# Performance work log

Measured on AMD Instinct MI355X. Metric: run time of the kernel, lower is better.

Reference implementation:

```python
import jax, jax.numpy as jnp
import numpy as np
from jax import lax


def _conv(x, w, b):
    # NCHW x OIHW, stride 1, VALID padding (matches nn.Conv2d padding=0)
    y = lax.conv_general_dilated(x, w, (1, 1), 'VALID',
                                 dimension_numbers=('NCHW', 'OIHW', 'NCHW'))
    return y + b[None, :, None, None]


def _maxpool2(x):
    return lax.reduce_window(x, -jnp.inf, lax.max, (1, 1, 2, 2), (1, 1, 2, 2), 'VALID')


def setup_inputs() -> dict:
    key = jax.random.key(0)
    ks = jax.random.split(key, 8)
    B, C, H, W = 4096, 3, 32, 32
    E, NC = 8, 1000  # out_dim (=n learners), num_classes
    inp = {
        'x': jax.random.normal(ks[0], (B, C, H, W), jnp.float32),
        'conv1_w': jax.random.normal(ks[1], (1, 3, 5, 5), jnp.float32) * 0.1,
        'conv1_b': jnp.zeros((1,), jnp.float32),
        'conv2_w': jax.random.normal(ks[2], (2, 1, 5, 5), jnp.float32) * 0.1,
        'conv2_b': jnp.zeros((2,), jnp.float32),
        'conv3_w': jax.random.normal(ks[3], (4, 2, 5, 5), jnp.float32) * 0.1,
        'conv3_b': jnp.zeros((4,), jnp.float32),
        'fc_w': jax.random.normal(ks[4], (E, 4), jnp.float32) * 0.5,
        'fc_b': jnp.zeros((E,), jnp.float32),
        'ens_w': jax.random.normal(ks[5], (E, C * H * W, NC), jnp.float32) * 0.02,
        'ens_b': jnp.zeros((E, NC), jnp.float32),
        'k': 2,
    }
    return inp


def reference(x, conv1_w, conv1_b, conv2_w, conv2_b, conv3_w, conv3_b,
              fc_w, fc_b, ens_w, ens_b, k):
    B = x.shape[0]
    # --- selector CNN stem ---
    h = jax.nn.relu(_conv(x, conv1_w, conv1_b))   # [B,1,28,28]
    h = _maxpool2(h)                              # [B,1,14,14]
    h = jax.nn.relu(_conv(h, conv2_w, conv2_b))   # [B,2,10,10]
    h = _maxpool2(h)                              # [B,2,5,5]
    h = jax.nn.relu(_conv(h, conv3_w, conv3_b))   # [B,4,1,1]
    h = h.reshape(B, -1)                          # [B,4]
    z = h @ fc_w.T + fc_b                         # [B,E]
    # L2NormalizationLayer with clamp(min=1e-9)
    z = z / jnp.clip(jnp.linalg.norm(z, axis=-1, keepdims=True), 1e-9, None)
    # TopK -> one-hot routing mask (straight-through style forward)
    _, idx = lax.top_k(z, k)                      # [B,k]
    mask = jax.nn.one_hot(idx, z.shape[-1], dtype=z.dtype).sum(-2)  # [B,E] in {0,1}
    # --- frozen ensemble: linear weak learners, combined via mask ---
    xf = x.reshape(B, -1)                          # [B,F]
    outs = jnp.einsum('bf,efc->bec', xf, ens_w) + ens_b[None]  # [B,E,NC]
    return (outs * mask[:, :, None]).sum(axis=1)   # [B,NC]
```

## Files before the change

kernel.cpp:

```cpp
#include <hip/hip_runtime.h>
#include <hip/hip_bf16.h>
#include <stdint.h>

#define B_SZ 4096
#define F_SZ 3072
#define NCLS 1000
#define NE 8
#define NPAD 1024
#define CAP 4096

#define OFF_CNT   0
#define OFF_LIST  1024
#define OFF_PAIR  132096
#define OFF_XB    262144
#define OFF_WT    25427968

typedef unsigned short u16;
typedef __attribute__((ext_vector_type(8))) short short8v;
typedef __attribute__((ext_vector_type(4))) float f32x4;

__device__ __forceinline__ u16 f2bf(float f) {
  unsigned int u = __float_as_uint(f);
  u = (u + 0x7FFFu + ((u >> 16) & 1u)) >> 16;
  return (u16)u;
}

__device__ __forceinline__ void gll16(const void* g, void* l) {
  __builtin_amdgcn_global_load_lds(
      (const __attribute__((address_space(1))) void*)g,
      (__attribute__((address_space(3))) void*)l, 16, 0, 0);
}

__global__ __launch_bounds__(256) void transpose_w(const float* __restrict__ ensw,
                                                   u16* __restrict__ wt) {
  __shared__ u16 tile[64 * 68];
  int t = threadIdx.x;
  int n0 = blockIdx.x * 64, k0 = blockIdx.y * 64, e = blockIdx.z;
  const float* src = ensw + (size_t)e * (F_SZ * NCLS);
  int kr = t >> 4, nq = (t & 15) * 4;
  for (int it = 0; it < 4; ++it) {
    int kk = kr + it * 16;
    const float* sp = src + (size_t)(k0 + kk) * NCLS + n0 + nq;
    float4 v;
    if (n0 + nq + 3 < NCLS) v = *(const float4*)sp;
    else {
      v.x = (n0 + nq     < NCLS) ? sp[0] : 0.f;
      v.y = (n0 + nq + 1 < NCLS) ? sp[1] : 0.f;
      v.z = (n0 + nq + 2 < NCLS) ? sp[2] : 0.f;
      v.w = (n0 + nq + 3 < NCLS) ? sp[3] : 0.f;
    }
    u16* d = tile + kk * 68 + nq;
    d[0] = f2bf(v.x); d[1] = f2bf(v.y); d[2] = f2bf(v.z); d[3] = f2bf(v.w);
  }
  __syncthreads();
  int rn = t >> 3, c8 = t & 7;
  for (int it = 0; it < 2; ++it) {
    int n = rn + it * 32;
    u16 o[8];
#pragma unroll
    for (int jj = 0; jj < 8; ++jj) o[jj] = tile[(c8 * 8 + jj) * 68 + n];
    uint4 pk;
    pk.x = (unsigned)o[0] | ((unsigned)o[1] << 16);
    pk.y = (unsigned)o[2] | ((unsigned)o[3] << 16);
    pk.z = (unsigned)o[4] | ((unsigned)o[5] << 16);
    pk.w = (unsigned)o[6] | ((unsigned)o[7] << 16);
    *(uint4*)(wt + ((size_t)(e * NPAD + n0 + n)) * F_SZ + k0 + c8 * 8) = pk;
  }
}

__global__ __launch_bounds__(128) void selector(
    const float* __restrict__ x,
    const float* __restrict__ w1, const float* __restrict__ b1,
    const float* __restrict__ w2, const float* __restrict__ b2,
    const float* __restrict__ w3, const float* __restrict__ b3,
    const float* __restrict__ fw, const float* __restrict__ fb,
    u16* __restrict__ xb16, int* __restrict__ cnt, int* __restrict__ list,
    int* __restrict__ expair) {
  __shared__ float wgt[384];
  __shared__ float S[2][4352];
  int t = threadIdx.x;
  for (int i = t; i < 372; i += 128) {
    float v;
    if      (i <  75) v = w1[i];
    else if (i <  76) v = b1[i - 75];
    else if (i < 126) v = w2[i - 76];
    else if (i < 128) v = b2[i - 126];
    else if (i < 328) v = w3[i - 128];
    else if (i < 332) v = b3[i - 328];
    else if (i < 364) v = fw[i - 332];
    else              v = fb[i - 364];
    wgt[i] = v;
  }
  int w = t >> 6, l = t & 63;
  int b = blockIdx.x * 2 + w;
  float* xs   = S[w];
  float* buf1 = xs + 3072;
  float* p1   = xs + 3856;
  float* buf2 = xs + 4052;
  float* p2   = xs + 4252;
  float* hb   = xs + 4302;
  float* zb   = xs + 4306;

  const float4* gx = (const float4*)(x + (size_t)b * F_SZ);
  float4* xs4 = (float4*)xs;
  ushort4* gxb = (ushort4*)(xb16 + (size_t)b * F_SZ);
  for (int it = 0; it < 12; ++it) {
    int idx = it * 64 + l;
    float4 v = gx[idx];
    xs4[idx] = v;
    ushort4 h4;
    h4.x = f2bf(v.x); h4.y = f2bf(v.y); h4.z = f2bf(v.z); h4.w = f2bf(v.w);
    gxb[idx] = h4;
  }
  __syncthreads();

  if (l < 56) {
    int y = l >> 1, xh = l & 1;
    float acc[14];
#pragma unroll
    for (int xc = 0; xc < 14; ++xc) acc[xc] = wgt[75];
    for (int c = 0; c < 3; ++c)
      for (int i = 0; i < 5; ++i) {
        const float4* rb = (const float4*)(xs + c * 1024 + (y + i) * 32) + xh * 3;
        float a[20];
#pragma unroll
        for (int q = 0; q < 5; ++q) {
          float4 v = rb[q];
          a[q * 4] = v.x; a[q * 4 + 1] = v.y; a[q * 4 + 2] = v.z; a[q * 4 + 3] = v.w;
        }
        if (xh) {
#pragma unroll
          for (int q = 0; q < 18; ++q) a[q] = a[q + 2];
        }
        const float* wp = wgt + c * 25 + i * 5;
        float W0 = wp[0], W1 = wp[1], W2 = wp[2], W3 = wp[3], W4 = wp[4];
#pragma unroll
        for (int xc = 0; xc < 14; ++xc)
          acc[xc] += a[xc] * W0 + a[xc + 1] * W1 + a[xc + 2] * W2 + a[xc + 3] * W3 + a[xc + 4] * W4;
      }
#pragma unroll
    for (int xc = 0; xc < 14; ++xc) buf1[y * 28 + xh * 14 + xc] = fmaxf(acc[xc], 0.f);
  }
  __syncthreads();

  for (int it = 0; it < 4; ++it) {
    int p = it * 64 + l;
    if (p < 196) {
      int py = p / 14, px = p % 14;
      const float* r0 = buf1 + (2 * py) * 28 + 2 * px;
      p1[p] = fmaxf(fmaxf(r0[0], r0[1]), fmaxf(r0[28], r0[29]));
    }
  }
  __syncthreads();

  for (int it = 0; it < 4; ++it) {
    int p = it * 64 + l;
    if (p < 200) {
      int o = p / 100, rem = p % 100, yy = rem / 10, xx = rem % 10;
      float acc = wgt[126 + o];
      const float* wp = wgt + 76 + o * 25;
      for (int i = 0; i < 5; ++i)
#pragma unroll
        for (int j = 0; j < 5; ++j) acc += p1[(yy + i) * 14 + xx + j] * wp[i * 5 + j];
      buf2[p] = fmaxf(acc, 0.f);
    }
  }
  __syncthreads();

  if (l < 50) {
    int o = l / 25, rem = l % 25, yy = rem / 5, xx = rem % 5;
    const float* r0 = buf2 + o * 100 + (2 * yy) * 10 + 2 * xx;
    p2[l] = fmaxf(fmaxf(r0[0], r0[1]), fmaxf(r0[10], r0[11]));
  }
  __syncthreads();

  if (l < 4) {
    float acc = wgt[328 + l];
    const float* wp = wgt + 128 + l * 50;
    for (int cc = 0; cc < 50; ++cc) acc += p2[cc] * wp[cc];
    hb[l] = fmaxf(acc, 0.f);
  }
  __syncthreads();

  if (l < 8) {
    float acc = wgt[364 + l];
    const float* wp = wgt + 332 + l * 4;
#pragma unroll
    for (int j = 0; j < 4; ++j) acc += hb[j] * wp[j];
    zb[l] = acc;
  }
  __syncthreads();

  if (l == 0) {
    float zz[8];
#pragma unroll
    for (int e = 0; e < 8; ++e) zz[e] = zb[e];
    int e1 = 0; float v1 = zz[0];
    for (int e = 1; e < 8; ++e) if (zz[e] > v1) { v1 = zz[e]; e1 = e; }
    int e2 = -1; float v2 = 0.f;
    for (int e = 0; e < 8; ++e) {
      if (e == e1) continue;
      if (e2 < 0 || zz[e] > v2) { v2 = zz[e]; e2 = e; }
    }
    int p1i = atomicAdd(&cnt[e1], 1); list[e1 * CAP + p1i] = b;
    int p2i = atomicAdd(&cnt[e2], 1); list[e2 * CAP + p2i] = b;
    expair[b] = e1 | (e2 << 8);
  }
}

__global__ __launch_bounds__(256) void bias_init(const int* __restrict__ expair,
                                                 const float* __restrict__ ensb,
                                                 float* __restrict__ out) {
  int b = blockIdx.x;
  int pr = expair[b];
  const float* p1 = ensb + (size_t)(pr & 255) * NCLS;
  const float* p2 = ensb + (size_t)((pr >> 8) & 255) * NCLS;
  float* op = out + (size_t)b * NCLS;
  for (int c = threadIdx.x; c < NCLS; c += 256) op[c] = p1[c] + p2[c];
}

__global__ __launch_bounds__(256) void moe_gemm(const u16* __restrict__ xb,
                                                const u16* __restrict__ wt,
                                                const int* __restrict__ cnt,
                                                const int* __restrict__ list,
                                                float* __restrict__ out) {
  __shared__ u16 As[128 * 32];
  __shared__ u16 Bs[128 * 32];
  __shared__ int idx_s[128];
  int e = blockIdx.z;
  int cnt_e = cnt[e];
  int m0 = blockIdx.y * 128;
  if (m0 >= cnt_e) return;
  int n0 = blockIdx.x * 128;
  int t = threadIdx.x;
  const int* lst = list + e * CAP;
  if (t < 128) {
    int m = m0 + t;
    idx_s[t] = lst[min(m, cnt_e - 1)];
  }
  __syncthreads();

  int rA1 = t >> 2,        sA1 = (t & 3) ^ ((rA1 >> 1) & 3);
  int rA2 = 64 + (t >> 2), sA2 = (t & 3) ^ ((rA2 >> 1) & 3);
  size_t ia1 = (size_t)idx_s[rA1], ia2 = (size_t)idx_s[rA2];
  const u16* pA1 = xb + ia1 * F_SZ + sA1 * 8;
  const u16* pA2 = xb + ia2 * F_SZ + sA2 * 8;
  const u16* pB1 = wt + ((size_t)(e * NPAD) + n0 + rA1) * F_SZ + sA1 * 8;
  const u16* pB2 = wt + ((size_t)(e * NPAD) + n0 + rA2) * F_SZ + sA2 * 8;
  u16* dA1 = As + t * 8;
  u16* dA2 = As + (t + 256) * 8;
  u16* dB1 = Bs + t * 8;
  u16* dB2 = Bs + (t + 256) * 8;

  int w = t >> 6, l = t & 63;
  int lr = l & 15, hk = l >> 4;
  int wrow = (w >> 1) * 64, wcol = (w & 1) * 64;
  const short8v* fA[4];
  const short8v* fB[4];
#pragma unroll
  for (int i = 0; i < 4; ++i) {
    int ra = wrow + i * 16 + lr;
    fA[i] = (const short8v*)(As + ra * 32 + (hk ^ ((ra >> 1) & 3)) * 8);
    int rb = wcol + i * 16 + lr;
    fB[i] = (const short8v*)(Bs + rb * 32 + (hk ^ ((rb >> 1) & 3)) * 8);
  }

  f32x4 acc[4][4] = {};
  for (int k0 = 0; k0 < F_SZ; k0 += 32) {
    __syncthreads();
    gll16(pA1, dA1); gll16(pA2, dA2);
    gll16(pB1, dB1); gll16(pB2, dB2);
    pA1 += 32; pA2 += 32; pB1 += 32; pB2 += 32;
    __syncthreads();
    short8v av[4], bv[4];
#pragma unroll
    for (int i = 0; i < 4; ++i) av[i] = *fA[i];
#pragma unroll
    for (int j = 0; j < 4; ++j) bv[j] = *fB[j];
#pragma unroll
    for (int i = 0; i < 4; ++i)
#pragma unroll
      for (int j = 0; j < 4; ++j)
        acc[i][j] = __builtin_amdgcn_mfma_f32_16x16x32_bf16(av[i], bv[j], acc[i][j], 0, 0, 0);
  }

#pragma unroll
  for (int i = 0; i < 4; ++i) {
#pragma unroll
    for (int r = 0; r < 4; ++r) {
      int mt = wrow + i * 16 + hk * 4 + r;
      if (m0 + mt < cnt_e) {
        float* orow = out + (size_t)idx_s[mt] * NCLS;
#pragma unroll
        for (int j = 0; j < 4; ++j) {
          int col = n0 + wcol + j * 16 + lr;
          if (col < NCLS) unsafeAtomicAdd(orow + col, acc[i][j][r]);
        }
      }
    }
  }
}

extern "C" void kernel_launch(void* const* d_in, const int* in_sizes, int n_in,
                              void* d_out, int out_size, void* d_ws, size_t ws_size,
                              hipStream_t stream) {
  const float* x   = (const float*)d_in[0];
  const float* w1  = (const float*)d_in[1];
  const float* b1  = (const float*)d_in[2];
  const float* w2  = (const float*)d_in[3];
  const float* b2  = (const float*)d_in[4];
  const float* w3  = (const float*)d_in[5];
  const float* b3  = (const float*)d_in[6];
  const float* fw  = (const float*)d_in[7];
  const float* fb  = (const float*)d_in[8];
  const float* ensw = (const float*)d_in[9];
  const float* ensb = (const float*)d_in[10];
  float* out = (float*)d_out;

  uint8_t* ws = (uint8_t*)d_ws;
  int* cnt    = (int*)(ws + OFF_CNT);
  int* list   = (int*)(ws + OFF_LIST);
  int* expair = (int*)(ws + OFF_PAIR);
  u16* xb16   = (u16*)(ws + OFF_XB);
  u16* wt     = (u16*)(ws + OFF_WT);

  hipMemsetAsync(cnt, 0, 64, stream);
  transpose_w<<<dim3(16, 48, 8), 256, 0, stream>>>(ensw, wt);
  selector<<<2048, 128, 0, stream>>>(x, w1, b1, w2, b2, w3, b3, fw, fb,
                                     xb16, cnt, list, expair);
  bias_init<<<4096, 256, 0, stream>>>(expair, ensb, out);
  moe_gemm<<<dim3(8, 32, 8), 256, 0, stream>>>(xb16, wt, cnt, list, out);
}
```

Baseline: 470.9 us.

## Double-buffer MoE GEMM with BK=64, pad selector smem rows, vectorize bias init

The MoE GEMM now keeps two LDS buffers with a K-tile of 64 and an XOR swizzle over 8 chunks. Global-to-LDS loads for the next stage are issued before the MFMAs on the current stage, and there is one barrier per iteration instead of two. The selector pads each image row to 36 floats in shared memory to reduce bank conflicts in the conv1 reads. Bias init switches to float4 loads and stores. The larger LDS footprint (64KB per GEMM block) may reduce occupancy.

```diff
diff --git a/kernel.cpp b/kernel.cpp
--- a/kernel.cpp
+++ b/kernel.cpp
@@ -68,6 +68,8 @@
   }
 }
 
+#define XST 36
+#define XCH 1152
 __global__ __launch_bounds__(128) void selector(
     const float* __restrict__ x,
     const float* __restrict__ w1, const float* __restrict__ b1,
@@ -77,7 +79,7 @@
     u16* __restrict__ xb16, int* __restrict__ cnt, int* __restrict__ list,
     int* __restrict__ expair) {
   __shared__ float wgt[384];
-  __shared__ float S[2][4352];
+  __shared__ float S[2][4704];
   int t = threadIdx.x;
   for (int i = t; i < 372; i += 128) {
     float v;
@@ -94,20 +96,21 @@
   int w = t >> 6, l = t & 63;
   int b = blockIdx.x * 2 + w;
   float* xs   = S[w];
-  float* buf1 = xs + 3072;
-  float* p1   = xs + 3856;
-  float* buf2 = xs + 4052;
-  float* p2   = xs + 4252;
-  float* hb   = xs + 4302;
-  float* zb   = xs + 4306;
+  float* buf1 = xs + 3456;
+  float* p1   = xs + 4240;
+  float* buf2 = xs + 4436;
+  float* p2   = xs + 4636;
+  float* hb   = xs + 4686;
+  float* zb   = xs + 4690;
 
   const float4* gx = (const float4*)(x + (size_t)b * F_SZ);
-  float4* xs4 = (float4*)xs;
   ushort4* gxb = (ushort4*)(xb16 + (size_t)b * F_SZ);
   for (int it = 0; it < 12; ++it) {
     int idx = it * 64 + l;
     float4 v = gx[idx];
-    xs4[idx] = v;
+    int f = idx * 4;
+    int c = f >> 10, rem = f & 1023, y = rem >> 5, xc = rem & 31;
+    *(float4*)(xs + c * XCH + y * XST + xc) = v;
     ushort4 h4;
     h4.x = f2bf(v.x); h4.y = f2bf(v.y); h4.z = f2bf(v.z); h4.w = f2bf(v.w);
     gxb[idx] = h4;
@@ -121,7 +124,7 @@
     for (int xc = 0; xc < 14; ++xc) acc[xc] = wgt[75];
     for (int c = 0; c < 3; ++c)
       for (int i = 0; i < 5; ++i) {
-        const float4* rb = (const float4*)(xs + c * 1024 + (y + i) * 32) + xh * 3;
+        const float4* rb = (const float4*)(xs + c * XCH + (y + i) * XST) + xh * 3;
         float a[20];
 #pragma unroll
         for (int q = 0; q < 5; ++q) {
@@ -212,11 +215,15 @@
                                                  const float* __restrict__ ensb,
                                                  float* __restrict__ out) {
   int b = blockIdx.x;
+  int t = threadIdx.x;
+  if (t >= 250) return;
   int pr = expair[b];
-  const float* p1 = ensb + (size_t)(pr & 255) * NCLS;
-  const float* p2 = ensb + (size_t)((pr >> 8) & 255) * NCLS;
-  float* op = out + (size_t)b * NCLS;
-  for (int c = threadIdx.x; c < NCLS; c += 256) op[c] = p1[c] + p2[c];
+  const float4* p1 = (const float4*)(ensb + (size_t)(pr & 255) * NCLS);
+  const float4* p2 = (const float4*)(ensb + (size_t)((pr >> 8) & 255) * NCLS);
+  float4* op = (float4*)(out + (size_t)b * NCLS);
+  float4 a = p1[t], c = p2[t];
+  float4 r; r.x = a.x + c.x; r.y = a.y + c.y; r.z = a.z + c.z; r.w = a.w + c.w;
+  op[t] = r;
 }
 
 __global__ __launch_bounds__(256) void moe_gemm(const u16* __restrict__ xb,
@@ -224,8 +231,8 @@
                                                 const int* __restrict__ cnt,
                                                 const int* __restrict__ list,
                                                 float* __restrict__ out) {
-  __shared__ u16 As[128 * 32];
-  __shared__ u16 Bs[128 * 32];
+  __shared__ u16 As[2][8192];
+  __shared__ u16 Bs[2][8192];
   __shared__ int idx_s[128];
   int e = blockIdx.z;
   int cnt_e = cnt[e];
@@ -234,54 +241,65 @@
   int n0 = blockIdx.x * 128;
   int t = threadIdx.x;
   const int* lst = list + e * CAP;
-  if (t < 128) {
-    int m = m0 + t;
-    idx_s[t] = lst[min(m, cnt_e - 1)];
-  }
-  __syncthreads();
-
-  int rA1 = t >> 2,        sA1 = (t & 3) ^ ((rA1 >> 1) & 3);
-  int rA2 = 64 + (t >> 2), sA2 = (t & 3) ^ ((rA2 >> 1) & 3);
-  size_t ia1 = (size_t)idx_s[rA1], ia2 = (size_t)idx_s[rA2];
-  const u16* pA1 = xb + ia1 * F_SZ + sA1 * 8;
-  const u16* pA2 = xb + ia2 * F_SZ + sA2 * 8;
-  const u16* pB1 = wt + ((size_t)(e * NPAD) + n0 + rA1) * F_SZ + sA1 * 8;
-  const u16* pB2 = wt + ((size_t)(e * NPAD) + n0 + rA2) * F_SZ + sA2 * 8;
-  u16* dA1 = As + t * 8;
-  u16* dA2 = As + (t + 256) * 8;
-  u16* dB1 = Bs + t * 8;
-  u16* dB2 = Bs + (t + 256) * 8;
+  if (t < 128) idx_s[t] = lst[min(m0 + t, cnt_e - 1)];
+  __syncthreads();
+
+  int tr = t >> 3;
+  int ts = t & 7;
+  int g  = ts ^ (tr & 7);
+  const u16* pA[4]; const u16* pB[4]; int ldst[4];
+#pragma unroll
+  for (int q = 0; q < 4; ++q) {
+    int row = q * 32 + tr;
+    pA[q] = xb + (size_t)idx_s[row] * F_SZ + g * 8;
+    pB[q] = wt + ((size_t)(e * NPAD + n0 + row)) * F_SZ + g * 8;
+    ldst[q] = (q * 256 + t) * 8;
+  }
 
   int w = t >> 6, l = t & 63;
   int lr = l & 15, hk = l >> 4;
   int wrow = (w >> 1) * 64, wcol = (w & 1) * 64;
-  const short8v* fA[4];
-  const short8v* fB[4];
+  int rA[4], rB[4];
 #pragma unroll
   for (int i = 0; i < 4; ++i) {
-    int ra = wrow + i * 16 + lr;
-    fA[i] = (const short8v*)(As + ra * 32 + (hk ^ ((ra >> 1) & 3)) * 8);
-    int rb = wcol + i * 16 + lr;
-    fB[i] = (const short8v*)(Bs + rb * 32 + (hk ^ ((rb >> 1) & 3)) * 8);
-  }
+    rA[i] = (wrow + i * 16 + lr) * 64;
+    rB[i] = (wcol + i * 16 + lr) * 64;
+  }
+  int sw0 = ((hk    ) ^ (lr & 7)) * 8;
+  int sw1 = ((hk + 4) ^ (lr & 7)) * 8;
+
+#pragma unroll
+  for (int q = 0; q < 4; ++q) { gll16(pA[q], &As[0][ldst[q]]); pA[q] += 64; }
+#pragma unroll
+  for (int q = 0; q < 4; ++q) { gll16(pB[q], &Bs[0][ldst[q]]); pB[q] += 64; }
+  __syncthreads();
 
   f32x4 acc[4][4] = {};
-  for (int k0 = 0; k0 < F_SZ; k0 += 32) {
+  for (int s = 0; s < 48; ++s) {
+    int cur = s & 1;
+    if (s < 47) {
+      int nxt = cur ^ 1;
+#pragma unroll
+      for (int q = 0; q < 4; ++q) { gll16(pA[q], &As[nxt][ldst[q]]); pA[q] += 64; }
+#pragma unroll
+      for (int q = 0; q < 4; ++q) { gll16(pB[q], &Bs[nxt][ldst[q]]); pB[q] += 64; }
+    }
+    short8v av[2][4], bv[2][4];
+#pragma unroll
+    for (int i = 0; i < 4; ++i) {
+      av[0][i] = *(const short8v*)(&As[cur][rA[i] + sw0]);
+      av[1][i] = *(const short8v*)(&As[cur][rA[i] + sw1]);
+      bv[0][i] = *(const short8v*)(&Bs[cur][rB[i] + sw0]);
+      bv[1][i] = *(const short8v*)(&Bs[cur][rB[i] + sw1]);
+    }
+#pragma unroll
+    for (int h = 0; h < 2; ++h)
+#pragma unroll
+      for (int i = 0; i < 4; ++i)
+#pragma unroll
+        for (int j = 0; j < 4; ++j)
+          acc[i][j] = __builtin_amdgcn_mfma_f32_16x16x32_bf16(av[h][i], bv[h][j], acc[i][j], 0, 0, 0);
     __syncthreads();
-    gll16(pA1, dA1); gll16(pA2, dA2);
-    gll16(pB1, dB1); gll16(pB2, dB2);
-    pA1 += 32; pA2 += 32; pB1 += 32; pB2 += 32;
-    __syncthreads();
-    short8v av[4], bv[4];
-#pragma unroll
-    for (int i = 0; i < 4; ++i) av[i] = *fA[i];
-#pragma unroll
-    for (int j = 0; j < 4; ++j) bv[j] = *fB[j];
-#pragma unroll
-    for (int i = 0; i < 4; ++i)
-#pragma unroll
-      for (int j = 0; j < 4; ++j)
-        acc[i][j] = __builtin_amdgcn_mfma_f32_16x16x32_bf16(av[i], bv[j], acc[i][j], 0, 0, 0);
   }
 
 #pragma unroll
```

New measurement: 483.2 us. 1.03x slower.
